# Kernel optimization log

Hardware: AMD Instinct MI355X
Metric: run time of the kernel (lower is better)

## Reference

```python
import jax, jax.numpy as jnp
import numpy as np

NEAR_THRESHOLD = 0.25
N = 1536          # entities (== max_entities)
D = 768           # d_model
H = 64            # classifier hidden width
NTYPES = 4        # relation types: 0=NEAR, 1=APPROACHING, 2=FLEEING, 3=ABOVE
SPATIAL = 8       # geometric feature dim


def setup_inputs() -> dict:
    key = jax.random.key(0)
    ks = jax.random.split(key, 6)
    entity_embeddings = jax.random.normal(ks[0], (N, D), dtype=jnp.float32)
    positions = jax.random.uniform(ks[1], (N, 3), dtype=jnp.float32)
    prev_positions = jax.random.uniform(ks[2], (N, 3), dtype=jnp.float32)
    in_dim = 2 * D + SPATIAL
    W1 = jax.random.normal(ks[3], (in_dim, H), dtype=jnp.float32) * (1.0 / np.sqrt(in_dim))
    b1 = jnp.zeros((H,), dtype=jnp.float32)
    W2 = jax.random.normal(ks[4], (H, NTYPES), dtype=jnp.float32) * (1.0 / np.sqrt(H))
    b2 = jnp.zeros((NTYPES,), dtype=jnp.float32)
    return {"entity_embeddings": entity_embeddings, "positions": positions,
            "prev_positions": prev_positions, "W1": W1, "b1": b1, "W2": W2, "b2": b2}


def reference(entity_embeddings, positions, prev_positions, W1, b1, W2, b2):
    n, d = entity_embeddings.shape
    velocities = positions - prev_positions
    # pairwise geometry: entry [i, j] corresponds to pair (a=i, b=j)
    rel_pos = positions[None, :, :] - positions[:, None, :]      # (N, N, 3) = pos_b - pos_a
    rel_vel = velocities[None, :, :] - velocities[:, None, :]    # (N, N, 3)
    distance = jnp.linalg.norm(rel_pos, axis=-1)                 # (N, N)
    closing = -(rel_pos * rel_vel).sum(-1) / jnp.maximum(distance, 1e-6)
    vdiff = rel_pos[..., 1]
    # spatial feats = [dx, dy, dz, dist, dvx, dvy, dvz, vertical_diff]
    sp = jnp.concatenate([rel_pos, distance[..., None], rel_vel, vdiff[..., None]], axis=-1)  # (N, N, 8)

    # first Linear on concat([emb_a, emb_b, sp]) decomposed into three projections
    W1a, W1b, W1s = W1[:d], W1[d:2 * d], W1[2 * d:]
    ha = entity_embeddings @ W1a                                  # (N, H)
    hb = entity_embeddings @ W1b                                  # (N, H)
    hidden = jax.nn.relu(ha[:, None, :] + hb[None, :, :]
                         + jnp.einsum('ijs,sh->ijh', sp, W1s) + b1)  # (N, N, H)
    logits = hidden @ W2 + b2                                     # (N, N, 4)
    probs = jax.nn.softmax(logits, axis=-1)
    best_idx = jnp.argmax(probs, axis=-1)
    conf = jnp.max(probs, axis=-1)

    # conditional overrides (same priority order as _classify_pair)
    near = distance < NEAR_THRESHOLD
    appr = ~near & (closing > 0.05)
    flee = ~near & ~appr & (closing < -0.05)
    above = ~near & ~appr & ~flee & (jnp.abs(vdiff) > 0.3) & (distance < 0.5)
    rel_type = jnp.where(near, 0,
               jnp.where(appr, 1,
               jnp.where(flee, 2,
               jnp.where(above, 3, best_idx)))).astype(jnp.int32)
    conf_out = jnp.where(near, jnp.maximum(conf, 0.8),
               jnp.where(appr, jnp.maximum(conf, 0.6),
               jnp.where(flee, jnp.maximum(conf, 0.6),
               jnp.where(above, jnp.maximum(conf, 0.5), conf))))

    upper = jnp.triu(jnp.ones((n, n), dtype=bool), k=1)           # i < j pairs only
    valid = upper & (conf_out > 0.3)
    return rel_type, conf_out, valid
```

## Files before the change

kernel.cpp:

```cpp
#include <hip/hip_runtime.h>

typedef float f4 __attribute__((ext_vector_type(4)));
typedef float f2 __attribute__((ext_vector_type(2)));

#define N 1536
#define D 768
#define H 64
#define NN (N * N)

static __device__ __forceinline__ f2 pk_add_sl(f2 a, f2 b) {
    f2 d; asm("v_pk_add_f32 %0, %1, %2 op_sel:[0,0] op_sel_hi:[0,1]"
              : "=v"(d) : "v"(a), "v"(b)); return d;
}
static __device__ __forceinline__ f2 pk_add_sh(f2 a, f2 b) {
    f2 d; asm("v_pk_add_f32 %0, %1, %2 op_sel:[1,0] op_sel_hi:[1,1]"
              : "=v"(d) : "v"(a), "v"(b)); return d;
}
static __device__ __forceinline__ f2 pk_fma(f2 a, f2 b, f2 c) {
    f2 d; asm("v_pk_fma_f32 %0, %1, %2, %3"
              : "=v"(d) : "v"(a), "v"(b), "v"(c)); return d;
}
static __device__ __forceinline__ void pk_fma_acc_sl(f2& acc, f2 a, f2 b) {
    asm("v_pk_fma_f32 %0, %1, %2, %0 op_sel:[0,0,0] op_sel_hi:[1,0,1]"
        : "+v"(acc) : "v"(a), "v"(b));
}
static __device__ __forceinline__ void pk_fma_acc_sh(f2& acc, f2 a, f2 b) {
    asm("v_pk_fma_f32 %0, %1, %2, %0 op_sel:[0,1,0] op_sel_hi:[1,1,1]"
        : "+v"(acc) : "v"(a), "v"(b));
}

__global__ __launch_bounds__(128) void k1_gemm(
    const float* __restrict__ E, const float* __restrict__ pos,
    const float* __restrict__ ppos, const float* __restrict__ W1,
    const float* __restrict__ b1, float* __restrict__ P, int KC)
{
    __shared__ float Es[8][192];

    const int tid = threadIdx.x;
    const int i0  = blockIdx.x * 8;
    const int kcc = blockIdx.y;
    const int k0  = kcc * KC;

    const int hg  = tid & 31;
    const int h0  = hg * 4;
    const int mat = h0 >> 6;
    const int hc  = h0 & 63;
    const int rp  = tid >> 5;
    const float* Wbase = W1 + (size_t)(mat * D + k0) * H + hc;

    f4 acc0 = {0.f, 0.f, 0.f, 0.f};
    f4 acc1 = {0.f, 0.f, 0.f, 0.f};

    for (int ks = 0; ks < KC; ks += 192) {
        if (ks) __syncthreads();
        for (int f = tid; f < 8 * 48; f += 128) {
            int row = f / 48, c = f - row * 48;
            *(f4*)&Es[row][c * 4] =
                *(const f4*)&E[(size_t)(i0 + row) * D + k0 + ks + c * 4];
        }
        __syncthreads();

        const float* Wc  = Wbase + (size_t)ks * H;
        const float* e0p = Es[2 * rp];
        const float* e1p = Es[2 * rp + 1];
        for (int kk = 0; kk < 192; kk += 8) {
#pragma unroll
            for (int u = 0; u < 8; ++u) {
                f4 w = *(const f4*)&Wc[(size_t)(kk + u) * H];
                float e0 = e0p[kk + u], e1 = e1p[kk + u];
                acc0 = __builtin_elementwise_fma((f4){e0, e0, e0, e0}, w, acc0);
                acc1 = __builtin_elementwise_fma((f4){e1, e1, e1, e1}, w, acc1);
            }
        }
    }

    if (kcc == 0) {
        const float* Ws = W1 + (size_t)2 * D * H + hc;
        f4 wp0 = *(const f4*)&Ws[0 * H];
        f4 wp1 = *(const f4*)&Ws[1 * H] + *(const f4*)&Ws[7 * H];
        f4 wp2 = *(const f4*)&Ws[2 * H];
        f4 wv0 = *(const f4*)&Ws[4 * H];
        f4 wv1 = *(const f4*)&Ws[5 * H];
        f4 wv2 = *(const f4*)&Ws[6 * H];
        f4 bb  = *(const f4*)&b1[hc];
#pragma unroll
        for (int r = 0; r < 2; ++r) {
            int i = i0 + 2 * rp + r;
            float px = pos[3 * i], py = pos[3 * i + 1], pz = pos[3 * i + 2];
            float vx = px - ppos[3 * i];
            float vy = py - ppos[3 * i + 1];
            float vz = pz - ppos[3 * i + 2];
            f4 g = px * wp0 + py * wp1 + pz * wp2 + vx * wv0 + vy * wv1 + vz * wv2;
            f4 add = (mat == 0) ? (bb - g) : g;
            if (r == 0) acc0 += add; else acc1 += add;
        }
    }

#pragma unroll
    for (int r = 0; r < 2; ++r) {
        int i = i0 + 2 * rp + r;
        f4 a = r ? acc1 : acc0;
#pragma unroll
        for (int c = 0; c < 4; ++c)
            P[(size_t)(kcc * 128 + h0 + c) * N + i] = a[c];
    }
}

__global__ __launch_bounds__(256) void k1b_reduce(
    const float* __restrict__ P, float* __restrict__ AB, int nkc)
{
    int idx = blockIdx.x * 256 + threadIdx.x;
    f4 s = {0.f, 0.f, 0.f, 0.f};
    for (int kc = 0; kc < nkc; ++kc)
        s += *(const f4*)&P[(size_t)kc * 128 * N + (size_t)idx * 4];
    *(f4*)&AB[(size_t)idx * 4] = s;
}

__global__ __launch_bounds__(128) void k2_main(
    const float* __restrict__ AB, const float* __restrict__ W1,
    const float* __restrict__ W2, const float* __restrict__ b2,
    const float* __restrict__ pos, const float* __restrict__ ppos,
    float* __restrict__ out)
{
    __shared__ float As[64][32];
    __shared__ float Bs[64][32];
    __shared__ float pis[32][3], vis[32][3], pjs[32][3], vjs[32][3];
    __shared__ f2 W2d[64][2];
    __shared__ f2 w3d[64];

    const int tid = threadIdx.x;
    const int i0 = blockIdx.y * 32;
    const int j0 = blockIdx.x * 32;

#pragma unroll
    for (int g = 0; g < 4; ++g) {
        int f = g * 128 + tid;
        int h = f >> 3, c = f & 7;
        *(f4*)&As[h][c * 4] = *(const f4*)&AB[(size_t)h * N + i0 + c * 4];
        *(f4*)&Bs[h][c * 4] = *(const f4*)&AB[(size_t)(64 + h) * N + j0 + c * 4];
    }
    if (tid < 32) {
        int i = i0 + tid;
        float px = pos[3 * i], py = pos[3 * i + 1], pz = pos[3 * i + 2];
        pis[tid][0] = px; pis[tid][1] = py; pis[tid][2] = pz;
        vis[tid][0] = px - ppos[3 * i];
        vis[tid][1] = py - ppos[3 * i + 1];
        vis[tid][2] = pz - ppos[3 * i + 2];
    } else if (tid < 64) {
        int t = tid - 32;
        int j = j0 + t;
        float px = pos[3 * j], py = pos[3 * j + 1], pz = pos[3 * j + 2];
        pjs[t][0] = px; pjs[t][1] = py; pjs[t][2] = pz;
        vjs[t][0] = px - ppos[3 * j];
        vjs[t][1] = py - ppos[3 * j + 1];
        vjs[t][2] = pz - ppos[3 * j + 2];
    } else {
        int t = tid - 64;
        f4 w2r = *(const f4*)&W2[t * 4];
        W2d[t][0] = (f2){w2r.x, w2r.y};
        W2d[t][1] = (f2){w2r.z, w2r.w};
        float w3h = W1[(size_t)(2 * D + 3) * H + t];
        w3d[t] = (f2){w3h, w3h};
    }
    __syncthreads();

    const int tx = tid & 15;
    const int ty = tid >> 4;

    f2 dd[4], dyv[4], clv[4];
    {
#pragma clang fp contract(off)
#pragma unroll
        for (int a = 0; a < 4; ++a) {
#pragma unroll
            for (int b = 0; b < 2; ++b) {
                int il = ty * 4 + a, jl = tx * 2 + b;
                float dx = pjs[jl][0] - pis[il][0];
                float dy = pjs[jl][1] - pis[il][1];
                float dz = pjs[jl][2] - pis[il][2];
                float s = dx * dx;
                s = s + dy * dy;
                s = s + dz * dz;
                float d = sqrtf(s);
                float rvx = vjs[jl][0] - vis[il][0];
                float rvy = vjs[jl][1] - vis[il][1];
                float rvz = vjs[jl][2] - vis[il][2];
                float dot = dx * rvx;
                dot = dot + dy * rvy;
                dot = dot + dz * rvz;
                float cl = -dot / fmaxf(d, 1e-6f);
                dd[a][b] = d; dyv[a][b] = dy; clv[a][b] = cl;
            }
        }
    }

    f2 acc[4][4];
#pragma unroll
    for (int a = 0; a < 4; ++a)
#pragma unroll
        for (int l = 0; l < 4; ++l)
            acc[a][l] = (f2){0.f, 0.f};

#pragma unroll 4
    for (int h = 0; h < 64; ++h) {
        f2 A01 = *(const f2*)&As[h][ty * 4];
        f2 A23 = *(const f2*)&As[h][ty * 4 + 2];
        f2 B2  = *(const f2*)&Bs[h][tx * 2];
        f2 w3v = w3d[h];
        f2 w2p01 = W2d[h][0];
        f2 w2p23 = W2d[h][1];
#pragma unroll
        for (int a = 0; a < 4; ++a) {
            f2 Ap = (a < 2) ? A01 : A23;
            f2 pre = (a & 1) ? pk_add_sh(Ap, B2) : pk_add_sl(Ap, B2);
            f2 hid = __builtin_elementwise_max(pk_fma(dd[a], w3v, pre),
                                               (f2){0.f, 0.f});
            pk_fma_acc_sl(acc[a][0], hid, w2p01);
            pk_fma_acc_sh(acc[a][1], hid, w2p01);
            pk_fma_acc_sl(acc[a][2], hid, w2p23);
            pk_fma_acc_sh(acc[a][3], hid, w2p23);
        }
    }

    const f4 B2v = *(const f4*)b2;

#pragma unroll
    for (int a = 0; a < 4; ++a) {
        int i = i0 + ty * 4 + a;
        f2 rt2, cf2, vl2;
#pragma unroll
        for (int b = 0; b < 2; ++b) {
            int j = j0 + tx * 2 + b;
            float l0 = acc[a][0][b] + B2v.x;
            float l1 = acc[a][1][b] + B2v.y;
            float l2 = acc[a][2][b] + B2v.z;
            float l3 = acc[a][3][b] + B2v.w;
            float mx = l0; int bidx = 0;
            if (l1 > mx) { mx = l1; bidx = 1; }
            if (l2 > mx) { mx = l2; bidx = 2; }
            if (l3 > mx) { mx = l3; bidx = 3; }
            float s = expf(l0 - mx);
            s += expf(l1 - mx);
            s += expf(l2 - mx);
            s += expf(l3 - mx);
            float conf = 1.0f / s;

            float d  = dd[a][b];
            float dy = dyv[a][b];
            float cl = clv[a][b];
            bool near = d < 0.25f;
            bool appr = !near && (cl > 0.05f);
            bool flee = !near && !appr && (cl < -0.05f);
            bool above = !near && !appr && !flee && (fabsf(dy) > 0.3f) && (d < 0.5f);
            int rt = near ? 0 : appr ? 1 : flee ? 2 : above ? 3 : bidx;
            float co = near  ? fmaxf(conf, 0.8f)
                     : appr  ? fmaxf(conf, 0.6f)
                     : flee  ? fmaxf(conf, 0.6f)
                     : above ? fmaxf(conf, 0.5f)
                             : conf;
            float vd = ((j > i) && (co > 0.3f)) ? 1.0f : 0.0f;
            rt2[b] = (float)rt;
            cf2[b] = co;
            vl2[b] = vd;
        }
        int col = j0 + tx * 2;
        *(f2*)&out[(size_t)i * N + col]                  = rt2;
        *(f2*)&out[(size_t)NN + (size_t)i * N + col]     = cf2;
        *(f2*)&out[(size_t)2 * NN + (size_t)i * N + col] = vl2;
    }
}

extern "C" void kernel_launch(void* const* d_in, const int* in_sizes, int n_in,
                              void* d_out, int out_size, void* d_ws, size_t ws_size,
                              hipStream_t stream)
{
    const float* E    = (const float*)d_in[0];
    const float* pos  = (const float*)d_in[1];
    const float* ppos = (const float*)d_in[2];
    const float* W1   = (const float*)d_in[3];
    const float* b1   = (const float*)d_in[4];
    const float* W2   = (const float*)d_in[5];
    const float* b2   = (const float*)d_in[6];
    float* out = (float*)d_out;
    float* P   = (float*)d_ws;

    const size_t part_sz = (size_t)4 * 128 * N;
    const size_t ab_sz   = (size_t)128 * N;
    int nkc = (ws_size >= (part_sz + ab_sz) * sizeof(float)) ? 4 : 1;
    int KC  = D / nkc;

    dim3 g1(N / 8, nkc);
    k1_gemm<<<g1, 128, 0, stream>>>(E, pos, ppos, W1, b1, P, KC);

    const float* AB;
    if (nkc > 1) {
        float* ABw = P + part_sz;
        k1b_reduce<<<(128 * N / 4) / 256, 256, 0, stream>>>(P, ABw, nkc);
        AB = ABw;
    } else {
        AB = P;
    }

    dim3 g2(N / 32, N / 32);
    k2_main<<<g2, 128, 0, stream>>>(AB, W1, W2, b2, pos, ppos, out);
}
```

Before: 128.2 us.

## Transpose k2 shared tiles, read W2/w3 from global, drop inline packed asm

Stores the A and B hidden-projection tiles in shared memory transposed and padded, so each thread fetches the A values for two h steps with wide f4 loads instead of several f2 loads. The W2 and w3 weight columns are no longer staged in shared memory and are read directly from global memory, which should be uniform across the block and so eligible for scalar loads. The hand-written v_pk_* inline asm is replaced with compiler elementwise builtins, and the loop now handles two h values per iteration. This relies on the compiler to emit packed FMAs with scalar operand broadcasting; if it does not, the inner loop may gain extra moves.

```diff
diff --git a/kernel.cpp b/kernel.cpp
--- a/kernel.cpp
+++ b/kernel.cpp
@@ -7,27 +7,6 @@
 #define D 768
 #define H 64
 #define NN (N * N)
-
-static __device__ __forceinline__ f2 pk_add_sl(f2 a, f2 b) {
-    f2 d; asm("v_pk_add_f32 %0, %1, %2 op_sel:[0,0] op_sel_hi:[0,1]"
-              : "=v"(d) : "v"(a), "v"(b)); return d;
-}
-static __device__ __forceinline__ f2 pk_add_sh(f2 a, f2 b) {
-    f2 d; asm("v_pk_add_f32 %0, %1, %2 op_sel:[1,0] op_sel_hi:[1,1]"
-              : "=v"(d) : "v"(a), "v"(b)); return d;
-}
-static __device__ __forceinline__ f2 pk_fma(f2 a, f2 b, f2 c) {
-    f2 d; asm("v_pk_fma_f32 %0, %1, %2, %3"
-              : "=v"(d) : "v"(a), "v"(b), "v"(c)); return d;
-}
-static __device__ __forceinline__ void pk_fma_acc_sl(f2& acc, f2 a, f2 b) {
-    asm("v_pk_fma_f32 %0, %1, %2, %0 op_sel:[0,0,0] op_sel_hi:[1,0,1]"
-        : "+v"(acc) : "v"(a), "v"(b));
-}
-static __device__ __forceinline__ void pk_fma_acc_sh(f2& acc, f2 a, f2 b) {
-    asm("v_pk_fma_f32 %0, %1, %2, %0 op_sel:[0,1,0] op_sel_hi:[1,1,1]"
-        : "+v"(acc) : "v"(a), "v"(b));
-}
 
 __global__ __launch_bounds__(128) void k1_gemm(
     const float* __restrict__ E, const float* __restrict__ pos,
@@ -122,11 +101,9 @@
     const float* __restrict__ pos, const float* __restrict__ ppos,
     float* __restrict__ out)
 {
-    __shared__ float As[64][32];
-    __shared__ float Bs[64][32];
+    __shared__ float At[8][260];
+    __shared__ float Bt[16][130];
     __shared__ float pis[32][3], vis[32][3], pjs[32][3], vjs[32][3];
-    __shared__ f2 W2d[64][2];
-    __shared__ f2 w3d[64];
 
     const int tid = threadIdx.x;
     const int i0 = blockIdx.y * 32;
@@ -136,8 +113,11 @@
     for (int g = 0; g < 4; ++g) {
         int f = g * 128 + tid;
         int h = f >> 3, c = f & 7;
-        *(f4*)&As[h][c * 4] = *(const f4*)&AB[(size_t)h * N + i0 + c * 4];
-        *(f4*)&Bs[h][c * 4] = *(const f4*)&AB[(size_t)(64 + h) * N + j0 + c * 4];
+        f4 va = *(const f4*)&AB[(size_t)h * N + i0 + c * 4];
+        *(f4*)&At[c][h * 4] = va;
+        f4 vb = *(const f4*)&AB[(size_t)(64 + h) * N + j0 + c * 4];
+        *(f2*)&Bt[2 * c][h * 2]     = (f2){vb.x, vb.y};
+        *(f2*)&Bt[2 * c + 1][h * 2] = (f2){vb.z, vb.w};
     }
     if (tid < 32) {
         int i = i0 + tid;
@@ -154,13 +134,6 @@
         vjs[t][0] = px - ppos[3 * j];
         vjs[t][1] = py - ppos[3 * j + 1];
         vjs[t][2] = pz - ppos[3 * j + 2];
-    } else {
-        int t = tid - 64;
-        f4 w2r = *(const f4*)&W2[t * 4];
-        W2d[t][0] = (f2){w2r.x, w2r.y};
-        W2d[t][1] = (f2){w2r.z, w2r.w};
-        float w3h = W1[(size_t)(2 * D + 3) * H + t];
-        w3d[t] = (f2){w3h, w3h};
     }
     __syncthreads();
 
@@ -201,24 +174,42 @@
         for (int l = 0; l < 4; ++l)
             acc[a][l] = (f2){0.f, 0.f};
 
+    const float* w3p = W1 + (size_t)(2 * D + 3) * H;
+
 #pragma unroll 4
-    for (int h = 0; h < 64; ++h) {
-        f2 A01 = *(const f2*)&As[h][ty * 4];
-        f2 A23 = *(const f2*)&As[h][ty * 4 + 2];
-        f2 B2  = *(const f2*)&Bs[h][tx * 2];
-        f2 w3v = w3d[h];
-        f2 w2p01 = W2d[h][0];
-        f2 w2p23 = W2d[h][1];
+    for (int hh = 0; hh < 32; ++hh) {
+        const int h = hh * 2;
+        f4 A0 = *(const f4*)&At[ty][h * 4];
+        f4 A1 = *(const f4*)&At[ty][h * 4 + 4];
+        f4 Bp = *(const f4*)&Bt[tx][h * 2];
+        float w30 = w3p[h], w31 = w3p[h + 1];
+        f4 w2a = *(const f4*)&W2[h * 4];
+        f4 w2b = *(const f4*)&W2[h * 4 + 4];
+
+        f2 B20 = (f2){Bp.x, Bp.y};
+        f2 B21 = (f2){Bp.z, Bp.w};
+        f2 w3v0 = (f2){w30, w30};
+        f2 w3v1 = (f2){w31, w31};
 #pragma unroll
         for (int a = 0; a < 4; ++a) {
-            f2 Ap = (a < 2) ? A01 : A23;
-            f2 pre = (a & 1) ? pk_add_sh(Ap, B2) : pk_add_sl(Ap, B2);
-            f2 hid = __builtin_elementwise_max(pk_fma(dd[a], w3v, pre),
-                                               (f2){0.f, 0.f});
-            pk_fma_acc_sl(acc[a][0], hid, w2p01);
-            pk_fma_acc_sh(acc[a][1], hid, w2p01);
-            pk_fma_acc_sl(acc[a][2], hid, w2p23);
-            pk_fma_acc_sh(acc[a][3], hid, w2p23);
+            {
+                f2 pre = (f2){A0[a], A0[a]} + B20;
+                f2 hid = __builtin_elementwise_fma(dd[a], w3v0, pre);
+                hid = __builtin_elementwise_max(hid, (f2){0.f, 0.f});
+                acc[a][0] = __builtin_elementwise_fma(hid, (f2){w2a.x, w2a.x}, acc[a][0]);
+                acc[a][1] = __builtin_elementwise_fma(hid, (f2){w2a.y, w2a.y}, acc[a][1]);
+                acc[a][2] = __builtin_elementwise_fma(hid, (f2){w2a.z, w2a.z}, acc[a][2]);
+                acc[a][3] = __builtin_elementwise_fma(hid, (f2){w2a.w, w2a.w}, acc[a][3]);
+            }
+            {
+                f2 pre = (f2){A1[a], A1[a]} + B21;
+                f2 hid = __builtin_elementwise_fma(dd[a], w3v1, pre);
+                hid = __builtin_elementwise_max(hid, (f2){0.f, 0.f});
+                acc[a][0] = __builtin_elementwise_fma(hid, (f2){w2b.x, w2b.x}, acc[a][0]);
+                acc[a][1] = __builtin_elementwise_fma(hid, (f2){w2b.y, w2b.y}, acc[a][1]);
+                acc[a][2] = __builtin_elementwise_fma(hid, (f2){w2b.z, w2b.z}, acc[a][2]);
+                acc[a][3] = __builtin_elementwise_fma(hid, (f2){w2b.w, w2b.w}, acc[a][3]);
+            }
         }
     }
 
```

Result: faster. 122.6 us (-4.4%).
